# Kernel tuning notes

Measured on AMD Instinct MI355X. Metric: run time of the kernel, lower is better.

## Reference

```python
import jax, jax.numpy as jnp
import numpy as np

N = 50000      # nodes
E = 800000     # edges (avg degree 16)
IN = 256       # in_size
HID = 64       # hid_size
H = 4          # n_head
OUT = 64       # out_size


def setup_inputs() -> dict:
    key = jax.random.key(0)
    ks = jax.random.split(key, 16)
    g = lambda k, shp: jax.random.normal(k, shp, jnp.float32) * 0.1
    return {
        "features": jax.random.normal(ks[0], (N, IN), jnp.float32),
        "src": jax.random.randint(ks[1], (E,), 0, N, jnp.int32),
        "dst": jax.random.randint(ks[2], (E,), 0, N, jnp.int32),
        # layer 0: 256 -> 4 heads x 64
        "W0": g(ks[3], (IN, H * HID)), "al0": g(ks[4], (H, HID)), "ar0": g(ks[5], (H, HID)), "b0": g(ks[6], (H * HID,)),
        # layer 1: 256 -> 4 heads x 64
        "W1": g(ks[7], (H * HID, H * HID)), "al1": g(ks[8], (H, HID)), "ar1": g(ks[9], (H, HID)), "b1": g(ks[10], (H * HID,)),
        # layer 2: 256 -> 4 heads x 64, relu activation, mean over heads
        "W2": g(ks[11], (H * HID, H * OUT)), "al2": g(ks[12], (H, OUT)), "ar2": g(ks[13], (H, OUT)), "b2": g(ks[14], (H * OUT,)),
    }


def gat_conv(h, src, dst, W, al, ar, b, apply_relu):
    """DGL GATConv (eval mode, dropout off), residual identity since in == H*D."""
    n = h.shape[0]
    hh, dd = al.shape
    feat = (h @ W).reshape(n, hh, dd)                       # [N,H,D]
    el = jnp.einsum('nhd,hd->nh', feat, al)                 # [N,H]
    er = jnp.einsum('nhd,hd->nh', feat, ar)                 # [N,H]
    e = jax.nn.leaky_relu(el[src] + er[dst], negative_slope=0.2)  # [E,H]
    # segment softmax over incoming edges of each dst node
    m = jax.ops.segment_max(e, dst, num_segments=n)         # [N,H]
    ex = jnp.exp(e - m[dst])
    den = jax.ops.segment_sum(ex, dst, num_segments=n)      # [N,H]
    alpha = ex / den[dst]                                   # [E,H]
    rst = jax.ops.segment_sum(feat[src] * alpha[..., None], dst, num_segments=n)  # [N,H,D]
    rst = rst + h.reshape(n, hh, dd) + b.reshape(1, hh, dd)  # residual + bias
    return jax.nn.relu(rst) if apply_relu else rst


def reference(features, src, dst, W0, al0, ar0, b0, W1, al1, ar1, b1, W2, al2, ar2, b2):
    h = gat_conv(features, src, dst, W0, al0, ar0, b0, False).reshape(N, -1)
    h = gat_conv(h, src, dst, W1, al1, ar1, b1, False).reshape(N, -1)
    h = gat_conv(h, src, dst, W2, al2, ar2, b2, True).mean(axis=1)  # [N,OUT]
    return h
```

## Files before the change

kernel.cpp:

```cpp
#include <hip/hip_runtime.h>

#define NNODE 50000
#define NEDGE 800000
#define NH 4
#define DH 64
#define HD 256
#define PADN 50048
#define EPAD 64

typedef __attribute__((ext_vector_type(8))) short short8v;
typedef __attribute__((ext_vector_type(4))) float float4v;

static __device__ __forceinline__ float b2f(unsigned short u) {
  union { float f; unsigned v; } x; x.v = ((unsigned)u) << 16; return x.f;
}
static __device__ __forceinline__ unsigned short f2b(float f) {
  unsigned u = __builtin_bit_cast(unsigned, f);
  u += 0x7fff + ((u >> 16) & 1);
  return (unsigned short)(u >> 16);
}

__global__ __launch_bounds__(256) void k_prep(const float* __restrict__ W0,
                                              const float* __restrict__ W1,
                                              const float* __restrict__ W2,
                                              const float* __restrict__ al0,
                                              const float* __restrict__ ar0,
                                              const float* __restrict__ al1,
                                              const float* __restrict__ ar1,
                                              const float* __restrict__ al2,
                                              const float* __restrict__ ar2,
                                              unsigned short* __restrict__ F0,
                                              unsigned short* __restrict__ F1,
                                              unsigned short* __restrict__ F2,
                                              unsigned short* __restrict__ G0,
                                              unsigned short* __restrict__ G1,
                                              unsigned short* __restrict__ G2) {
  int L = blockIdx.y;
  const float* W = L == 0 ? W0 : (L == 1 ? W1 : W2);
  if (blockIdx.x < 32) {
    unsigned short* F = L == 0 ? F0 : (L == 1 ? F1 : F2);
    int idx = blockIdx.x * 256 + threadIdx.x;
    int lane = idx & 63;
    int ni = (idx >> 6) & 3;
    int head = (idx >> 8) & 3;
    int t = idx >> 10;
    int row = head * 64 + ni * 16 + (lane & 15);
    int kb = t * 32 + (lane >> 4) * 8;
    unsigned short v[8];
#pragma unroll
    for (int j = 0; j < 8; ++j) v[j] = f2b(W[(size_t)(kb + j) * HD + row]);
    *(short8v*)(F + (size_t)idx * 8) = *(const short8v*)v;
  } else {
    const float* al = L == 0 ? al0 : (L == 1 ? al1 : al2);
    const float* ar = L == 0 ? ar0 : (L == 1 ? ar1 : ar2);
    unsigned short* G = L == 0 ? G0 : (L == 1 ? G1 : G2);
    int k = threadIdx.x;
    const float* wr = W + (size_t)k * HD;
    float s[8] = {};
#pragma unroll
    for (int h = 0; h < 4; ++h)
#pragma unroll 4
      for (int dq = 0; dq < 16; ++dq) {
        float4v w4 = *(const float4v*)(wr + h * 64 + dq * 4);
        const float* alp = al + h * 64 + dq * 4;
        const float* arp = ar + h * 64 + dq * 4;
#pragma unroll
        for (int j = 0; j < 4; ++j) {
          s[h] = fmaf(w4[j], alp[j], s[h]);
          s[4 + h] = fmaf(w4[j], arp[j], s[4 + h]);
        }
      }
    int base = (k >> 5) * 512 + ((k >> 3) & 3) * 128 + (k & 7);
#pragma unroll
    for (int j = 0; j < 8; ++j) G[base + j * 8] = f2b(s[j]);
#pragma unroll
    for (int j = 8; j < 16; ++j) G[base + j * 8] = 0;
  }
}

__global__ void k_edge(const int* __restrict__ src, const int* __restrict__ dst,
                       int* __restrict__ fill, int* __restrict__ csrp) {
  int e = blockIdx.x * 256 + threadIdx.x;
  if (e < NEDGE) {
    int d = dst[e];
    int pos = atomicAdd(&fill[d], 1);
    if (pos < EPAD) csrp[(d << 6) + pos] = src[e];
  }
}

template <bool FP32A>
__global__ __launch_bounds__(256) void k_gemm(const float* __restrict__ Af,
                                              const unsigned short* __restrict__ Ab,
                                              const unsigned short* __restrict__ Wtf,
                                              const unsigned short* __restrict__ walrf,
                                              unsigned short* __restrict__ featb,
                                              float* __restrict__ el,
                                              float* __restrict__ er) {
  __shared__ unsigned short As[8][32][40];
  const int row0 = blockIdx.x * 32;
  const int tid = threadIdx.x;
  const int lane = tid & 63;
  const int head = tid >> 6;
  const int lr = lane & 15;
  const int kf = (lane >> 4) * 8;

  {
    const int r = tid >> 3, c = tid & 7;
    int grow = row0 + r;
    if (FP32A) {
      int gr = grow < NNODE ? grow : 0;
      const float* ap = Af + (size_t)gr * HD;
#pragma unroll
      for (int j = 0; j < 4; ++j) {
        int col8 = c + j * 8;
        float4v f0 = *(const float4v*)(ap + col8 * 8);
        float4v f1 = *(const float4v*)(ap + col8 * 8 + 4);
        uint4 pk;
        pk.x = (unsigned)f2b(f0.x) | ((unsigned)f2b(f0.y) << 16);
        pk.y = (unsigned)f2b(f0.z) | ((unsigned)f2b(f0.w) << 16);
        pk.z = (unsigned)f2b(f1.x) | ((unsigned)f2b(f1.y) << 16);
        pk.w = (unsigned)f2b(f1.z) | ((unsigned)f2b(f1.w) << 16);
        *(uint4*)&As[col8 >> 2][r][(col8 & 3) * 8] = pk;
      }
    } else {
      const unsigned short* ap = Ab + (size_t)grow * HD;
#pragma unroll
      for (int j = 0; j < 4; ++j) {
        int col8 = c + j * 8;
        *(uint4*)&As[col8 >> 2][r][(col8 & 3) * 8] = *(const uint4*)(ap + col8 * 8);
      }
    }
  }
  __syncthreads();

  float4v acc[2][4] = {};
  float4v acc_e = {};
  const bool do_e = head < 2;

  const unsigned short* wb = Wtf + (size_t)(head * 4 * 64 + lane) * 8;
  short8v bc[4], bn[4], be, ben;
#pragma unroll
  for (int ni = 0; ni < 4; ++ni) bc[ni] = *(const short8v*)(wb + ni * 512);
  if (do_e) be = *(const short8v*)(walrf + (size_t)lane * 8);

#pragma unroll
  for (int t = 0; t < 8; ++t) {
    if (t < 7) {
#pragma unroll
      for (int ni = 0; ni < 4; ++ni)
        bn[ni] = *(const short8v*)(wb + (size_t)(t + 1) * 8192 + ni * 512);
      if (do_e) ben = *(const short8v*)(walrf + (size_t)((t + 1) * 64 + lane) * 8);
    }
    short8v af[2];
#pragma unroll
    for (int mi = 0; mi < 2; ++mi)
      af[mi] = *(const short8v*)&As[t][mi * 16 + lr][kf];
#pragma unroll
    for (int mi = 0; mi < 2; ++mi)
#pragma unroll
      for (int ni = 0; ni < 4; ++ni)
        acc[mi][ni] = __builtin_amdgcn_mfma_f32_16x16x32_bf16(bc[ni], af[mi], acc[mi][ni], 0, 0, 0);
    if (do_e)
      acc_e = __builtin_amdgcn_mfma_f32_16x16x32_bf16(af[head & 1], be, acc_e, 0, 0, 0);
#pragma unroll
    for (int ni = 0; ni < 4; ++ni) bc[ni] = bn[ni];
    be = ben;
  }

  const int rg = (lane >> 4) * 4;

#pragma unroll
  for (int mi = 0; mi < 2; ++mi) {
    int node = row0 + mi * 16 + lr;
    if (node < NNODE) {
#pragma unroll
      for (int ni = 0; ni < 4; ++ni) {
        uint2 o;
        o.x = (unsigned)f2b(acc[mi][ni][0]) | ((unsigned)f2b(acc[mi][ni][1]) << 16);
        o.y = (unsigned)f2b(acc[mi][ni][2]) | ((unsigned)f2b(acc[mi][ni][3]) << 16);
        *(uint2*)(featb + (size_t)node * HD + head * 64 + ni * 16 + rg) = o;
      }
    }
  }

#pragma unroll
  for (int reg = 0; reg < 4; ++reg) {
    int grow = row0 + (head & 1) * 16 + rg + reg;
    if (do_e && grow < NNODE) {
      if (lr < 4) el[grow * NH + lr] = acc_e[reg];
      else if (lr < 8) er[grow * NH + lr - 4] = acc_e[reg];
    }
  }
}

template <int LAYER>
__global__ __launch_bounds__(256) void k_agg(const int* __restrict__ fillarr,
                                             const int* __restrict__ csrp,
                                             const float* __restrict__ el,
                                             const float* __restrict__ er,
                                             const unsigned short* __restrict__ featb,
                                             const unsigned short* __restrict__ hinb,
                                             const float* __restrict__ hinf,
                                             const float* __restrict__ bias,
                                             void* __restrict__ outv) {
  const int tid = threadIdx.x;
  const int w = tid >> 6;
  const int lane = tid & 63;
  const int n = blockIdx.x * 4 + w;
  const int e2 = lane >> 5;
  const int h = (lane >> 3) & 3;
  const int dg = lane & 7;
  const int deg = min(fillarr[n], EPAD);

  __shared__ float alpha_s[4][64][4];
  __shared__ int src_s[4][64];

  const float4v er4 = *(const float4v*)(er + n * 4);

  int s = 0;
  float4v lg = {-1e30f, -1e30f, -1e30f, -1e30f};
  if (lane < deg) {
    s = csrp[(n << 6) + lane];
    float4v e4 = *(const float4v*)(el + s * 4);
#pragma unroll
    for (int c = 0; c < 4; ++c) {
      float x = e4[c] + er4[c];
      lg[c] = x > 0.f ? x : 0.2f * x;
    }
  }
  float4v p;
#pragma unroll
  for (int c = 0; c < 4; ++c) p[c] = __expf(lg[c]);
  *(float4v*)&alpha_s[w][lane][0] = p;
  src_s[w][lane] = s;

  float acc[8] = {};
  float aden = 0.f;
  const int foff = (h << 6) + (dg << 3);
  int nit = (((deg + 1) >> 1) + 3) & ~3;
  for (int pj = 0; pj < nit; pj += 4) {
    float a[4];
    int sv[4];
    uint4 u[4];
#pragma unroll
    for (int q = 0; q < 4; ++q) {
      int e = ((pj + q) << 1) + e2;
      a[q] = alpha_s[w][e][h];
      sv[q] = src_s[w][e];
    }
#pragma unroll
    for (int q = 0; q < 4; ++q)
      u[q] = *(const uint4*)(featb + ((size_t)sv[q] << 8) + foff);
#pragma unroll
    for (int q = 0; q < 4; ++q) {
      aden += a[q];
      unsigned uu[4] = {u[q].x, u[q].y, u[q].z, u[q].w};
#pragma unroll
      for (int t = 0; t < 4; ++t) {
        float flo = __builtin_bit_cast(float, uu[t] << 16);
        float fhi = __builtin_bit_cast(float, uu[t] & 0xffff0000u);
        acc[2 * t] = fmaf(a[q], flo, acc[2 * t]);
        acc[2 * t + 1] = fmaf(a[q], fhi, acc[2 * t + 1]);
      }
    }
  }
#pragma unroll
  for (int k = 0; k < 8; ++k) acc[k] += __shfl_xor(acc[k], 32, 64);
  aden += __shfl_xor(aden, 32, 64);

  float inv = aden > 0.f ? 1.f / aden : 0.f;

  float hr[8];
  if (LAYER == 0) {
    const float4v* hp = (const float4v*)(hinf + ((size_t)n << 8) + foff);
    float4v h0 = hp[0], h1 = hp[1];
    hr[0] = h0.x; hr[1] = h0.y; hr[2] = h0.z; hr[3] = h0.w;
    hr[4] = h1.x; hr[5] = h1.y; hr[6] = h1.z; hr[7] = h1.w;
  } else {
    uint4 hv = *(const uint4*)(hinb + ((size_t)n << 8) + foff);
    unsigned hh[4] = {hv.x, hv.y, hv.z, hv.w};
#pragma unroll
    for (int k = 0; k < 8; ++k) {
      unsigned hu = (k & 1) ? (hh[k >> 1] & 0xffff0000u) : (hh[k >> 1] << 16);
      hr[k] = __builtin_bit_cast(float, hu);
    }
  }
  const float4v* bp = (const float4v*)(bias + foff);
  float4v bb0 = bp[0], bb1 = bp[1];
  float bb[8] = {bb0.x, bb0.y, bb0.z, bb0.w, bb1.x, bb1.y, bb1.z, bb1.w};
  float v[8];
#pragma unroll
  for (int k = 0; k < 8; ++k) v[k] = acc[k] * inv + hr[k] + bb[k];

  if (LAYER == 2) {
#pragma unroll
    for (int k = 0; k < 8; ++k) {
      v[k] = fmaxf(v[k], 0.f);
      v[k] += __shfl_xor(v[k], 8, 64);
      v[k] += __shfl_xor(v[k], 16, 64);
      v[k] *= 0.25f;
    }
    if (lane < 8) {
      float* out = (float*)outv + (size_t)n * DH + (dg << 3);
      *(float4v*)out = (float4v){v[0], v[1], v[2], v[3]};
      *(float4v*)(out + 4) = (float4v){v[4], v[5], v[6], v[7]};
    }
  } else {
    if (e2 == 0) {
      uint4 o;
      unsigned ov[4];
#pragma unroll
      for (int q = 0; q < 4; ++q)
        ov[q] = (unsigned)f2b(v[2 * q]) | ((unsigned)f2b(v[2 * q + 1]) << 16);
      o.x = ov[0]; o.y = ov[1]; o.z = ov[2]; o.w = ov[3];
      *(uint4*)((unsigned short*)outv + ((size_t)n << 8) + foff) = o;
    }
  }
}

extern "C" void kernel_launch(void* const* d_in, const int* in_sizes, int n_in,
                              void* d_out, int out_size, void* d_ws, size_t ws_size,
                              hipStream_t stream) {
  const float* features = (const float*)d_in[0];
  const int* src = (const int*)d_in[1];
  const int* dst = (const int*)d_in[2];
  const float* W0 = (const float*)d_in[3];
  const float* al0 = (const float*)d_in[4];
  const float* ar0 = (const float*)d_in[5];
  const float* b0 = (const float*)d_in[6];
  const float* W1 = (const float*)d_in[7];
  const float* al1 = (const float*)d_in[8];
  const float* ar1 = (const float*)d_in[9];
  const float* b1 = (const float*)d_in[10];
  const float* W2 = (const float*)d_in[11];
  const float* al2 = (const float*)d_in[12];
  const float* ar2 = (const float*)d_in[13];
  const float* b2 = (const float*)d_in[14];
  float* out = (float*)d_out;

  char* p = (char*)d_ws;
  auto carve = [&](size_t bytes) {
    char* q = p;
    p += (bytes + 255) & ~(size_t)255;
    return q;
  };
  unsigned short* h1b = (unsigned short*)carve((size_t)PADN * HD * 2);
  unsigned short* h2b = (unsigned short*)carve((size_t)PADN * HD * 2);
  unsigned short* featb = (unsigned short*)carve((size_t)PADN * HD * 2);
  unsigned short* wtf0 = (unsigned short*)carve((size_t)8192 * 8 * 2);
  unsigned short* wtf1 = (unsigned short*)carve((size_t)8192 * 8 * 2);
  unsigned short* wtf2 = (unsigned short*)carve((size_t)8192 * 8 * 2);
  unsigned short* walf0 = (unsigned short*)carve((size_t)8 * 512 * 2);
  unsigned short* walf1 = (unsigned short*)carve((size_t)8 * 512 * 2);
  unsigned short* walf2 = (unsigned short*)carve((size_t)8 * 512 * 2);
  float* el = (float*)carve((size_t)NNODE * NH * 4);
  float* er = (float*)carve((size_t)NNODE * NH * 4);
  int* fill = (int*)carve((size_t)NNODE * 4);
  int* csrp = (int*)carve((size_t)NNODE * EPAD * 4);

  hipMemsetAsync(fill, 0, (size_t)NNODE * 4, stream);

  k_prep<<<dim3(33, 3), 256, 0, stream>>>(W0, W1, W2, al0, ar0, al1, ar1, al2, ar2,
                                          wtf0, wtf1, wtf2, walf0, walf1, walf2);
  k_edge<<<NEDGE / 256, 256, 0, stream>>>(src, dst, fill, csrp);

  dim3 gg(PADN / 32);

  k_gemm<true><<<gg, 256, 0, stream>>>(features, nullptr, wtf0, walf0, featb, el, er);
  k_agg<0><<<NNODE / 4, 256, 0, stream>>>(fill, csrp, el, er, featb, nullptr, features, b0, h1b);

  k_gemm<false><<<gg, 256, 0, stream>>>(nullptr, h1b, wtf1, walf1, featb, el, er);
  k_agg<1><<<NNODE / 4, 256, 0, stream>>>(fill, csrp, el, er, featb, h1b, nullptr, b1, h2b);

  k_gemm<false><<<gg, 256, 0, stream>>>(nullptr, h2b, wtf2, walf2, featb, el, er);
  k_agg<2><<<NNODE / 4, 256, 0, stream>>>(fill, csrp, el, er, featb, h2b, nullptr, b2, (void*)out);
}
```

Baseline: 347.6 us.

## Store features head-major and split layer 0/1 aggregation per head

Node features and hidden activations move from node-major [N,256] to head-major [4][N,64] slices, so each head's gather rows are contiguous 128-byte blocks. The GEMM reads and writes the new layout. Layers 0 and 1 get a new aggregation kernel with a 2D grid over nodes and heads, where each wave handles one head and gathers 8 edges in parallel. The goal is better cache locality per head-slice gather and more parallelism, at the cost of redundant edge-score work across heads and a wider lane reduction.

```diff
diff --git a/kernel.cpp b/kernel.cpp
--- a/kernel.cpp
+++ b/kernel.cpp
@@ -7,6 +7,7 @@
 #define HD 256
 #define PADN 50048
 #define EPAD 64
+#define SLICE ((size_t)PADN * 64)
 
 typedef __attribute__((ext_vector_type(8))) short short8v;
 typedef __attribute__((ext_vector_type(4))) float float4v;
@@ -123,11 +124,12 @@
         *(uint4*)&As[col8 >> 2][r][(col8 & 3) * 8] = pk;
       }
     } else {
-      const unsigned short* ap = Ab + (size_t)grow * HD;
 #pragma unroll
       for (int j = 0; j < 4; ++j) {
         int col8 = c + j * 8;
-        *(uint4*)&As[col8 >> 2][r][(col8 & 3) * 8] = *(const uint4*)(ap + col8 * 8);
+        const unsigned short* ap =
+            Ab + (size_t)(col8 >> 3) * SLICE + (size_t)grow * 64 + (col8 & 7) * 8;
+        *(uint4*)&As[col8 >> 2][r][(col8 & 3) * 8] = *(const uint4*)ap;
       }
     }
   }
@@ -178,7 +180,7 @@
         uint2 o;
         o.x = (unsigned)f2b(acc[mi][ni][0]) | ((unsigned)f2b(acc[mi][ni][1]) << 16);
         o.y = (unsigned)f2b(acc[mi][ni][2]) | ((unsigned)f2b(acc[mi][ni][3]) << 16);
-        *(uint2*)(featb + (size_t)node * HD + head * 64 + ni * 16 + rg) = o;
+        *(uint2*)(featb + (size_t)head * SLICE + (size_t)node * 64 + ni * 16 + rg) = o;
       }
     }
   }
@@ -194,15 +196,111 @@
 }
 
 template <int LAYER>
-__global__ __launch_bounds__(256) void k_agg(const int* __restrict__ fillarr,
-                                             const int* __restrict__ csrp,
-                                             const float* __restrict__ el,
-                                             const float* __restrict__ er,
-                                             const unsigned short* __restrict__ featb,
-                                             const unsigned short* __restrict__ hinb,
-                                             const float* __restrict__ hinf,
-                                             const float* __restrict__ bias,
-                                             void* __restrict__ outv) {
+__global__ __launch_bounds__(256) void k_agg01(const int* __restrict__ fillarr,
+                                               const int* __restrict__ csrp,
+                                               const float* __restrict__ el,
+                                               const float* __restrict__ er,
+                                               const unsigned short* __restrict__ featb,
+                                               const unsigned short* __restrict__ hinb,
+                                               const float* __restrict__ hinf,
+                                               const float* __restrict__ bias,
+                                               unsigned short* __restrict__ outb) {
+  const int tid = threadIdx.x;
+  const int w = tid >> 6;
+  const int lane = tid & 63;
+  const int n = blockIdx.x * 4 + w;
+  const int h = blockIdx.y;
+  const int e8 = lane >> 3;
+  const int dg = lane & 7;
+  const int deg = min(fillarr[n], EPAD);
+
+  __shared__ uint2 as_s[4][64];
+
+  int s = 0;
+  float x = -1e30f;
+  if (lane < deg) {
+    s = csrp[(n << 6) + lane];
+    float e = el[s * NH + h] + er[n * NH + h];
+    x = e > 0.f ? e : 0.2f * e;
+  }
+  float pp = __expf(x);
+  uint2 pk;
+  pk.x = __builtin_bit_cast(unsigned, pp);
+  pk.y = (unsigned)s;
+  as_s[w][lane] = pk;
+
+  const unsigned short* fb = featb + (size_t)h * SLICE;
+  float acc[8] = {};
+  float aden = 0.f;
+  int ng = (deg + 7) >> 3;
+  ng = (ng + 1) & ~1;
+  for (int g = 0; g < ng; g += 2) {
+    uint2 v0 = as_s[w][g * 8 + e8];
+    uint2 v1 = as_s[w][(g + 1) * 8 + e8];
+    float a0 = __builtin_bit_cast(float, v0.x);
+    float a1 = __builtin_bit_cast(float, v1.x);
+    uint4 u0 = *(const uint4*)(fb + (size_t)v0.y * 64 + (dg << 3));
+    uint4 u1 = *(const uint4*)(fb + (size_t)v1.y * 64 + (dg << 3));
+    aden += a0 + a1;
+    unsigned uu0[4] = {u0.x, u0.y, u0.z, u0.w};
+    unsigned uu1[4] = {u1.x, u1.y, u1.z, u1.w};
+#pragma unroll
+    for (int t = 0; t < 4; ++t) {
+      acc[2 * t] = fmaf(a0, __builtin_bit_cast(float, uu0[t] << 16), acc[2 * t]);
+      acc[2 * t + 1] = fmaf(a0, __builtin_bit_cast(float, uu0[t] & 0xffff0000u), acc[2 * t + 1]);
+      acc[2 * t] = fmaf(a1, __builtin_bit_cast(float, uu1[t] << 16), acc[2 * t]);
+      acc[2 * t + 1] = fmaf(a1, __builtin_bit_cast(float, uu1[t] & 0xffff0000u), acc[2 * t + 1]);
+    }
+  }
+
+#pragma unroll
+  for (int off = 8; off < 64; off <<= 1) {
+#pragma unroll
+    for (int k = 0; k < 8; ++k) acc[k] += __shfl_xor(acc[k], off, 64);
+    aden += __shfl_xor(aden, off, 64);
+  }
+
+  if (e8 == 0) {
+    float inv = aden > 0.f ? 1.f / aden : 0.f;
+    float hr[8];
+    if (LAYER == 0) {
+      const float4v* hp = (const float4v*)(hinf + (size_t)n * HD + h * 64 + (dg << 3));
+      float4v h0 = hp[0], h1 = hp[1];
+      hr[0] = h0.x; hr[1] = h0.y; hr[2] = h0.z; hr[3] = h0.w;
+      hr[4] = h1.x; hr[5] = h1.y; hr[6] = h1.z; hr[7] = h1.w;
+    } else {
+      uint4 hv = *(const uint4*)(hinb + (size_t)h * SLICE + (size_t)n * 64 + (dg << 3));
+      unsigned hh[4] = {hv.x, hv.y, hv.z, hv.w};
+#pragma unroll
+      for (int k = 0; k < 8; ++k) {
+        unsigned hu = (k & 1) ? (hh[k >> 1] & 0xffff0000u) : (hh[k >> 1] << 16);
+        hr[k] = __builtin_bit_cast(float, hu);
+      }
+    }
+    const float4v* bp = (const float4v*)(bias + h * 64 + (dg << 3));
+    float4v bb0 = bp[0], bb1 = bp[1];
+    float bb[8] = {bb0.x, bb0.y, bb0.z, bb0.w, bb1.x, bb1.y, bb1.z, bb1.w};
+    uint4 o;
+    unsigned ov[4];
+#pragma unroll
+    for (int q = 0; q < 4; ++q) {
+      float va = acc[2 * q] * inv + hr[2 * q] + bb[2 * q];
+      float vb = acc[2 * q + 1] * inv + hr[2 * q + 1] + bb[2 * q + 1];
+      ov[q] = (unsigned)f2b(va) | ((unsigned)f2b(vb) << 16);
+    }
+    o.x = ov[0]; o.y = ov[1]; o.z = ov[2]; o.w = ov[3];
+    *(uint4*)(outb + (size_t)h * SLICE + (size_t)n * 64 + (dg << 3)) = o;
+  }
+}
+
+__global__ __launch_bounds__(256) void k_agg2(const int* __restrict__ fillarr,
+                                              const int* __restrict__ csrp,
+                                              const float* __restrict__ el,
+                                              const float* __restrict__ er,
+                                              const unsigned short* __restrict__ featb,
+                                              const unsigned short* __restrict__ hinb,
+                                              const float* __restrict__ bias,
+                                              float* __restrict__ out) {
   const int tid = threadIdx.x;
   const int w = tid >> 6;
   const int lane = tid & 63;
@@ -224,8 +322,8 @@
     float4v e4 = *(const float4v*)(el + s * 4);
 #pragma unroll
     for (int c = 0; c < 4; ++c) {
-      float x = e4[c] + er4[c];
-      lg[c] = x > 0.f ? x : 0.2f * x;
+      float xx = e4[c] + er4[c];
+      lg[c] = xx > 0.f ? xx : 0.2f * xx;
     }
   }
   float4v p;
@@ -236,7 +334,7 @@
 
   float acc[8] = {};
   float aden = 0.f;
-  const int foff = (h << 6) + (dg << 3);
+  const unsigned short* fb = featb + (size_t)h * SLICE;
   int nit = (((deg + 1) >> 1) + 3) & ~3;
   for (int pj = 0; pj < nit; pj += 4) {
     float a[4];
@@ -250,71 +348,45 @@
     }
 #pragma unroll
     for (int q = 0; q < 4; ++q)
-      u[q] = *(const uint4*)(featb + ((size_t)sv[q] << 8) + foff);
+      u[q] = *(const uint4*)(fb + (size_t)sv[q] * 64 + (dg << 3));
 #pragma unroll
     for (int q = 0; q < 4; ++q) {
       aden += a[q];
       unsigned uu[4] = {u[q].x, u[q].y, u[q].z, u[q].w};
 #pragma unroll
       for (int t = 0; t < 4; ++t) {
-        float flo = __builtin_bit_cast(float, uu[t] << 16);
-        float fhi = __builtin_bit_cast(float, uu[t] & 0xffff0000u);
-        acc[2 * t] = fmaf(a[q], flo, acc[2 * t]);
-        acc[2 * t + 1] = fmaf(a[q], fhi, acc[2 * t + 1]);
+        acc[2 * t] = fmaf(a[q], __builtin_bit_cast(float, uu[t] << 16), acc[2 * t]);
+        acc[2 * t + 1] = fmaf(a[q], __builtin_bit_cast(float, uu[t] & 0xffff0000u), acc[2 * t + 1]);
       }
     }
   }
 #pragma unroll
   for (int k = 0; k < 8; ++k) acc[k] += __shfl_xor(acc[k], 32, 64);
   aden += __shfl_xor(aden, 32, 64);
-
   float inv = aden > 0.f ? 1.f / aden : 0.f;
 
-  float hr[8];
-  if (LAYER == 0) {
-    const float4v* hp = (const float4v*)(hinf + ((size_t)n << 8) + foff);
-    float4v h0 = hp[0], h1 = hp[1];
-    hr[0] = h0.x; hr[1] = h0.y; hr[2] = h0.z; hr[3] = h0.w;
-    hr[4] = h1.x; hr[5] = h1.y; hr[6] = h1.z; hr[7] = h1.w;
-  } else {
-    uint4 hv = *(const uint4*)(hinb + ((size_t)n << 8) + foff);
-    unsigned hh[4] = {hv.x, hv.y, hv.z, hv.w};
-#pragma unroll
-    for (int k = 0; k < 8; ++k) {
-      unsigned hu = (k & 1) ? (hh[k >> 1] & 0xffff0000u) : (hh[k >> 1] << 16);
-      hr[k] = __builtin_bit_cast(float, hu);
-    }
-  }
-  const float4v* bp = (const float4v*)(bias + foff);
+  uint4 hv = *(const uint4*)(hinb + (size_t)h * SLICE + (size_t)n * 64 + (dg << 3));
+  unsigned hh[4] = {hv.x, hv.y, hv.z, hv.w};
+  const float4v* bp = (const float4v*)(bias + (h << 6) + (dg << 3));
   float4v bb0 = bp[0], bb1 = bp[1];
   float bb[8] = {bb0.x, bb0.y, bb0.z, bb0.w, bb1.x, bb1.y, bb1.z, bb1.w};
   float v[8];
 #pragma unroll
-  for (int k = 0; k < 8; ++k) v[k] = acc[k] * inv + hr[k] + bb[k];
-
-  if (LAYER == 2) {
-#pragma unroll
-    for (int k = 0; k < 8; ++k) {
-      v[k] = fmaxf(v[k], 0.f);
-      v[k] += __shfl_xor(v[k], 8, 64);
-      v[k] += __shfl_xor(v[k], 16, 64);
-      v[k] *= 0.25f;
-    }
-    if (lane < 8) {
-      float* out = (float*)outv + (size_t)n * DH + (dg << 3);
-      *(float4v*)out = (float4v){v[0], v[1], v[2], v[3]};
-      *(float4v*)(out + 4) = (float4v){v[4], v[5], v[6], v[7]};
-    }
-  } else {
-    if (e2 == 0) {
-      uint4 o;
-      unsigned ov[4];
-#pragma unroll
-      for (int q = 0; q < 4; ++q)
-        ov[q] = (unsigned)f2b(v[2 * q]) | ((unsigned)f2b(v[2 * q + 1]) << 16);
-      o.x = ov[0]; o.y = ov[1]; o.z = ov[2]; o.w = ov[3];
-      *(uint4*)((unsigned short*)outv + ((size_t)n << 8) + foff) = o;
-    }
+  for (int k = 0; k < 8; ++k) {
+    unsigned hu = (k & 1) ? (hh[k >> 1] & 0xffff0000u) : (hh[k >> 1] << 16);
+    v[k] = acc[k] * inv + __builtin_bit_cast(float, hu) + bb[k];
+  }
+#pragma unroll
+  for (int k = 0; k < 8; ++k) {
+    v[k] = fmaxf(v[k], 0.f);
+    v[k] += __shfl_xor(v[k], 8, 64);
+    v[k] += __shfl_xor(v[k], 16, 64);
+    v[k] *= 0.25f;
+  }
+  if (lane < 8) {
+    float* op = out + (size_t)n * DH + (dg << 3);
+    *(float4v*)op = (float4v){v[0], v[1], v[2], v[3]};
+    *(float4v*)(op + 4) = (float4v){v[4], v[5], v[6], v[7]};
   }
 }
 
@@ -365,13 +437,14 @@
   k_edge<<<NEDGE / 256, 256, 0, stream>>>(src, dst, fill, csrp);
 
   dim3 gg(PADN / 32);
+  dim3 ga01(NNODE / 4, NH);
 
   k_gemm<true><<<gg, 256, 0, stream>>>(features, nullptr, wtf0, walf0, featb, el, er);
-  k_agg<0><<<NNODE / 4, 256, 0, stream>>>(fill, csrp, el, er, featb, nullptr, features, b0, h1b);
+  k_agg01<0><<<ga01, 256, 0, stream>>>(fill, csrp, el, er, featb, nullptr, features, b0, h1b);
 
   k_gemm<false><<<gg, 256, 0, stream>>>(nullptr, h1b, wtf1, walf1, featb, el, er);
-  k_agg<1><<<NNODE / 4, 256, 0, stream>>>(fill, csrp, el, er, featb, h1b, nullptr, b1, h2b);
+  k_agg01<1><<<ga01, 256, 0, stream>>>(fill, csrp, el, er, featb, h1b, nullptr, b1, h2b);
 
   k_gemm<false><<<gg, 256, 0, stream>>>(nullptr, h2b, wtf2, walf2, featb, el, er);
-  k_agg<2><<<NNODE / 4, 256, 0, stream>>>(fill, csrp, el, er, featb, h2b, nullptr, b2, (void*)out);
-}
+  k_agg2<<<NNODE / 4, 256, 0, stream>>>(fill, csrp, el, er, featb, h2b, b2, out);
+}
```

Measured after the change: 382.3 us. 1.1x slower.
